# Kernel optimization log

Measured on AMD Instinct MI355X. Metric: run time of the kernel, lower is better.

The kernel has to match this reference:

```python
import jax, jax.numpy as jnp
import numpy as np

B, CIN, H, W = 4, 256, 56, 56
COUT, K = 256, 3
STRIDE, PAD, OG = 1, 1, 1
KK = K * K


def setup_inputs() -> dict:
    key = jax.random.key(0)
    k1, k2, k3, k4 = jax.random.split(key, 4)
    x = jax.random.normal(k1, (B, CIN, H, W), jnp.float32)
    # deformable conv weight [Cout, Cin/groups, K, K]
    weight = jax.random.normal(k2, (COUT, CIN, K, K), jnp.float32) * 0.05
    # offset-predicting 3x3 conv: 2*OG*K*K output channels (small init -> modest offsets)
    off_w = jax.random.normal(k3, (2 * OG * KK, CIN, 3, 3), jnp.float32) * 0.01
    off_b = jax.random.normal(k4, (2 * OG * KK,), jnp.float32) * 0.01
    return {"x": x, "weight": weight, "off_w": off_w, "off_b": off_b}


def _deform_conv(x, weight, off_w, off_b):
    Bn, C, Hh, Ww = x.shape
    # offset = param_generator(x): 3x3 conv, stride 1, pad 1
    offset = jax.lax.conv_general_dilated(
        x, off_w, window_strides=(1, 1), padding=((1, 1), (1, 1)),
        dimension_numbers=("NCHW", "OIHW", "NCHW")) + off_b[None, :, None, None]
    Ho = (Hh + 2 * PAD - K) // STRIDE + 1
    Wo = (Ww + 2 * PAD - K) // STRIDE + 1
    # torchvision layout: [B, OG, KK, (dy,dx), Ho, Wo]
    off = offset.reshape(Bn, OG, KK, 2, Ho, Wo)

    kh = jnp.arange(KK) // K
    kw = jnp.arange(KK) % K
    base_y = (jnp.arange(Ho) * STRIDE - PAD)[None, :, None] + kh[:, None, None]  # [KK,Ho,1]
    base_x = (jnp.arange(Wo) * STRIDE - PAD)[None, None, :] + kw[:, None, None]  # [KK,1,Wo]
    py = base_y[None, None].astype(x.dtype) + off[:, :, :, 0]  # [B,OG,KK,Ho,Wo]
    px = base_x[None, None].astype(x.dtype) + off[:, :, :, 1]

    Cg = C // OG
    xg = x.reshape(Bn, OG, Cg, Hh * Ww)

    def gather(yc, xc, wgt):
        # zero-padded bilinear corner: out-of-bounds samples contribute 0
        valid = (yc >= 0) & (yc < Hh) & (xc >= 0) & (xc < Ww)
        idx = (jnp.clip(yc, 0, Hh - 1) * Ww + jnp.clip(xc, 0, Ww - 1)).reshape(Bn, OG, 1, -1)
        v = jnp.take_along_axis(xg, idx, axis=3)            # [B,OG,Cg,KK*Ho*Wo]
        w = (wgt * valid.astype(wgt.dtype)).reshape(Bn, OG, 1, -1)
        return v * w

    y0 = jnp.floor(py).astype(jnp.int32)
    x0 = jnp.floor(px).astype(jnp.int32)
    ty = py - y0
    tx = px - x0
    sampled = (gather(y0,     x0,     (1 - ty) * (1 - tx))
             + gather(y0,     x0 + 1, (1 - ty) * tx)
             + gather(y0 + 1, x0,     ty * (1 - tx))
             + gather(y0 + 1, x0 + 1, ty * tx))
    sampled = sampled.reshape(Bn, C, KK, Ho, Wo)
    # weighted accumulation: implicit GEMM over (Cin, KK)
    return jnp.einsum("bikhw,oik->bohw", sampled, weight.reshape(COUT, C, KK))


def reference(x, weight, off_w, off_b):
    return _deform_conv(x, weight, off_w, off_b)
```

## Files before the change

kernel.cpp:

```cpp
#include <hip/hip_runtime.h>
#include <hip/hip_bf16.h>

#define B_N   4
#define CIN_  256
#define HH_   56
#define WW_   56
#define COUT_ 256
#define KK_   9
#define HW_   3136
#define KDIM  2304
#define NOFF  (B_N*18*HW_)
#define NOUT  (B_N*COUT_*HW_)

typedef __attribute__((ext_vector_type(8))) short short8;
typedef __attribute__((ext_vector_type(4))) float float4v;

__device__ __forceinline__ short f2bf_bits(float v) {
    union { __hip_bfloat16 h; short s; } u;
    u.h = __float2bfloat16(v);
    return u.s;
}
__device__ __forceinline__ float bfbits2f(short s) {
    union { unsigned u; float f; } u2;
    u2.u = ((unsigned)(unsigned short)s) << 16;
    return u2.f;
}

#define NB_AT  2304
#define NB_XT  784
#define NB_OW3 288
__global__ __launch_bounds__(256) void k_front(const float* __restrict__ x,
                                               const float* __restrict__ wgt,
                                               const float* __restrict__ ow,
                                               short* __restrict__ At2,
                                               short* __restrict__ xTb,
                                               short* __restrict__ owT3) {
    __shared__ float tile[64][65];
    int bx = blockIdx.x;
    int t = threadIdx.x;
    if (bx < NB_AT) {
        int i = bx*256 + t;
        int e = i & 7;
        int l = (i >> 3) & 63;
        int gg = i >> 9;
        int g  = gg % 72;
        int rt = gg / 72;
        int m = rt*16 + (l & 15);
        int k = g*32 + (l >> 4)*8 + e;
        int kk = k >> 8;  int ci = k & 255;
        At2[i] = f2bf_bits(wgt[(size_t)(m*CIN_ + ci)*9 + kk]);
        return;
    }
    if (bx < NB_AT + NB_XT) {
        int g = bx - NB_AT;
        int b = g / 196; int r = g % 196;
        int c0 = (r / 49) * 64; int p0 = (r % 49) * 64;
        int tp = t & 63;  int tc = t >> 6;
        #pragma unroll
        for (int i = 0; i < 16; ++i) {
            int ci = tc*16 + i;
            tile[ci][tp] = x[((size_t)b*CIN_ + c0 + ci)*HW_ + p0 + tp];
        }
        __syncthreads();
        #pragma unroll
        for (int i = 0; i < 16; ++i) {
            int p = tc*16 + i;
            xTb[((size_t)b*HW_ + p0 + p)*CIN_ + c0 + tp] = f2bf_bits(tile[tp][p]);
        }
        return;
    }
    {
        int i = (bx - NB_AT - NB_XT)*256 + t;
        int c = i / KDIM; int r = i % KDIM;
        int kk = r >> 8;  int ci = r & 255;
        owT3[i] = (c < 18) ? f2bf_bits(ow[(size_t)(c*CIN_ + ci)*9 + kk]) : 0;
    }
}

__global__ __launch_bounds__(256) void k_offgemm(const short* __restrict__ owT3,
                                                 const short* __restrict__ xTb,
                                                 float* __restrict__ pOff2) {
    __shared__ short sA[32*64];
    __shared__ short sB[64*64];
    __shared__ int   sP2[3*64];
    int t = threadIdx.x;
    int posb = blockIdx.x * 64;
    int b    = blockIdx.y;
    int ks   = blockIdx.z;
    int kt0  = ks * 768;
    int kend = kt0 + 768;

    for (int e = t; e < 3*64; e += 256) {
        int kk = ks*3 + (e >> 6); int row = e & 63;
        int pos = posb + row;
        int h = pos / WW_, w = pos % WW_;
        int yy = h + kk/3 - 1, xx = w + kk%3 - 1;
        bool v = (yy >= 0) && (yy < HH_) && (xx >= 0) && (xx < WW_);
        sP2[e] = v ? (yy*WW_ + xx) : -1;
    }
    __syncthreads();

    int arow = t >> 3,  aq  = t & 7;
    int brow = t >> 2,  bqc = (t & 3) * 2;

    int wv = t >> 6;
    int wm = (wv >> 1) * 16;
    int wn = (wv & 1) * 32;
    int lane = t & 63;
    int lm = lane & 15;
    int qd = lane >> 4;

    float4v acc[2];
    acc[0] = (float4v)(0.f); acc[1] = (float4v)(0.f);

    const short* gA = owT3 + (size_t)arow*KDIM + aq*8;
    const short* xb = xTb + (size_t)b*HW_*CIN_;

    short* wA = sA + (((arow >> 4)*8 + aq)*16 + ((arow + 2*aq) & 15))*8;
    short* wB[2];
    #pragma unroll
    for (int j = 0; j < 2; ++j) {
        int qq = bqc + j;
        wB[j] = sB + (((brow >> 4)*8 + qq)*16 + ((brow + 2*qq) & 15))*8;
    }

    short8 pa, pb[2];
    const short8 zero8 = (short8)(0);
    pa = *(const short8*)(gA + kt0);
    {
        int p2 = sP2[brow];
        #pragma unroll
        for (int j = 0; j < 2; ++j) {
            int ci0 = (kt0 & 255) + (bqc + j)*8;
            pb[j] = (p2 >= 0) ? *(const short8*)(xb + (size_t)p2*CIN_ + ci0) : zero8;
        }
    }

    for (int kt = kt0; kt < kend; kt += 64) {
        __syncthreads();
        *(short8*)wA = pa;
        #pragma unroll
        for (int j = 0; j < 2; ++j) *(short8*)wB[j] = pb[j];
        __syncthreads();
        int kt2 = kt + 64;
        if (kt2 < kend) {
            pa = *(const short8*)(gA + kt2);
            int kkl = (kt2 >> 8) - ks*3;
            int p2 = sP2[kkl*64 + brow];
            int cb = kt2 & 255;
            #pragma unroll
            for (int j = 0; j < 2; ++j) {
                int ci0 = cb + (bqc + j)*8;
                pb[j] = (p2 >= 0) ? *(const short8*)(xb + (size_t)p2*CIN_ + ci0) : zero8;
            }
        }
        #pragma unroll
        for (int kss = 0; kss < 2; ++kss) {
            int qe = kss*4 + qd;
            int sw = (lm + 2*qe) & 15;
            short8 af, bf[2];
            af = *(short8*)(sA + ((((wm>>4))*8 + qe)*16 + sw)*8);
            #pragma unroll
            for (int j = 0; j < 2; ++j)
                bf[j] = *(short8*)(sB + ((((wn>>4) + j)*8 + qe)*16 + sw)*8);
            #pragma unroll
            for (int j = 0; j < 2; ++j)
                acc[j] = __builtin_amdgcn_mfma_f32_16x16x32_bf16(
                             af, bf[j], acc[j], 0, 0, 0);
        }
    }

    float* pbase = pOff2 + (size_t)ks*NOFF;
    #pragma unroll
    for (int j = 0; j < 2; ++j) {
        int col = posb + wn + j*16 + lm;
        #pragma unroll
        for (int r = 0; r < 4; ++r) {
            int c = wm + qd*4 + r;
            if (c < 18)
                pbase[((size_t)(b*18 + c))*HW_ + col] = acc[j][r];
        }
    }
}

__global__ __launch_bounds__(256) void k_gemm(const short* __restrict__ At2,
                                              const short* __restrict__ xTb,
                                              const float* __restrict__ pOff2,
                                              const float* __restrict__ ob,
                                              float* __restrict__ pout) {
    __shared__ short sB[64*64];
    __shared__ int4   sPI[3*64];
    __shared__ float4 sPW[3*64];
    int t = threadIdx.x;

    int idx = blockIdx.x;
    int xcd = idx & 7;
    int b   = xcd & 3;
    int q   = (idx >> 3)*2 + (xcd >> 2);
    int m0   = (q & 1) * 128;
    int r2   = q >> 1;
    int posb = (r2 % 49) * 64;
    int ks   = r2 / 49;

    for (int e = t; e < 3*64; e += 256) {
        int kk = ks*3 + (e >> 6); int pl = e & 63;
        int pos = posb + pl;
        int h = pos / WW_, w = pos % WW_;
        size_t oy = (size_t)(b*18 + 2*kk    )*HW_ + pos;
        size_t ox = (size_t)(b*18 + 2*kk + 1)*HW_ + pos;
        float dy = ob[2*kk], dx = ob[2*kk + 1];
        #pragma unroll
        for (int s = 0; s < 3; ++s) {
            dy += pOff2[(size_t)s*NOFF + oy];
            dx += pOff2[(size_t)s*NOFF + ox];
        }
        float py = (float)(h - 1 + kk/3) + dy;
        float px = (float)(w - 1 + kk%3) + dx;
        float y0f = floorf(py), x0f = floorf(px);
        int y0 = (int)y0f, x0 = (int)x0f;
        float ty = py - y0f, tx = px - x0f;
        bool vy0 = (y0   >= 0) && (y0   < HH_);
        bool vy1 = (y0+1 >= 0) && (y0+1 < HH_);
        bool vx0 = (x0   >= 0) && (x0   < WW_);
        bool vx1 = (x0+1 >= 0) && (x0+1 < WW_);
        int y0c = min(max(y0,   0), HH_-1), y1c = min(max(y0+1, 0), HH_-1);
        int x0c = min(max(x0,   0), WW_-1), x1c = min(max(x0+1, 0), WW_-1);
        sPI[e] = make_int4(y0c*WW_+x0c, y0c*WW_+x1c, y1c*WW_+x0c, y1c*WW_+x1c);
        sPW[e] = make_float4((vy0 && vx0) ? (1.f-ty)*(1.f-tx) : 0.f,
                             (vy0 && vx1) ? (1.f-ty)*tx       : 0.f,
                             (vy1 && vx0) ? ty*(1.f-tx)       : 0.f,
                             (vy1 && vx1) ? ty*tx             : 0.f);
    }
    __syncthreads();

    int brow = t >> 2,  bqc = (t & 3) * 2;

    int wv = t >> 6;
    int wm = (wv >> 1) * 64;
    int wn = (wv & 1) * 32;
    int lane = t & 63;
    int lm = lane & 15;
    int qd = lane >> 4;

    float4v acc[4][2];
    #pragma unroll
    for (int i = 0; i < 4; ++i)
        #pragma unroll
        for (int j = 0; j < 2; ++j) acc[i][j] = (float4v)(0.f);

    const short* xb = xTb + (size_t)b*HW_*CIN_;
    const short* pA = At2 + (((size_t)((m0 + wm) >> 4) * 72) << 9) + (size_t)lane * 8;
    int g0 = ks * 24;

    short* wB[2];
    #pragma unroll
    for (int j = 0; j < 2; ++j) {
        int qq = bqc + j;
        wB[j] = sB + (((brow >> 4)*8 + qq)*16 + ((brow + 2*qq) & 15))*8;
    }

    short8 cg[2][4];
    float4 bwv;

#define CGLOAD(itX) do {                                                      \
    int4 id_ = sPI[((itX) >> 2)*64 + brow];                                   \
    bwv = sPW[((itX) >> 2)*64 + brow];                                        \
    int cb_ = ((itX) & 3) * 64;                                               \
    _Pragma("unroll")                                                         \
    for (int j = 0; j < 2; ++j) {                                             \
        int ci0_ = cb_ + (bqc + j)*8;                                         \
        cg[j][0] = *(const short8*)(xb + (size_t)id_.x*CIN_ + ci0_);          \
        cg[j][1] = *(const short8*)(xb + (size_t)id_.y*CIN_ + ci0_);          \
        cg[j][2] = *(const short8*)(xb + (size_t)id_.z*CIN_ + ci0_);          \
        cg[j][3] = *(const short8*)(xb + (size_t)id_.w*CIN_ + ci0_);          \
    }                                                                         \
} while (0)

    CGLOAD(0);

    for (int it = 0; it < 12; ++it) {
        short8 af[8];
        #pragma unroll
        for (int kss = 0; kss < 2; ++kss)
            #pragma unroll
            for (int i = 0; i < 4; ++i)
                af[kss*4 + i] = *(const short8*)(
                    pA + ((size_t)(i*72 + g0 + it*2 + kss) << 9));

        short8 pk[2];
        #pragma unroll
        for (int j = 0; j < 2; ++j) {
            float f[8];
            #pragma unroll
            for (int e = 0; e < 8; ++e)
                f[e] = bwv.x*bfbits2f(cg[j][0][e]) + bwv.y*bfbits2f(cg[j][1][e])
                     + bwv.z*bfbits2f(cg[j][2][e]) + bwv.w*bfbits2f(cg[j][3][e]);
            union { short8 s8; __hip_bfloat162 h2[4]; } pu;
            #pragma unroll
            for (int e2 = 0; e2 < 4; ++e2)
                pu.h2[e2] = __float22bfloat162_rn(make_float2(f[2*e2], f[2*e2+1]));
            pk[j] = pu.s8;
        }
        __syncthreads();
        #pragma unroll
        for (int j = 0; j < 2; ++j) *(short8*)wB[j] = pk[j];
        __syncthreads();
        if (it + 1 < 12) CGLOAD(it + 1);

        #pragma unroll
        for (int kss = 0; kss < 2; ++kss) {
            int qe = kss*4 + qd;
            int sw = (lm + 2*qe) & 15;
            short8 bf[2];
            #pragma unroll
            for (int j = 0; j < 2; ++j)
                bf[j] = *(short8*)(sB + ((((wn>>4) + j)*8 + qe)*16 + sw)*8);
            #pragma unroll
            for (int i = 0; i < 4; ++i)
                #pragma unroll
                for (int j = 0; j < 2; ++j)
                    acc[i][j] = __builtin_amdgcn_mfma_f32_16x16x32_bf16(
                                    af[kss*4 + i], bf[j], acc[i][j], 0, 0, 0);
        }
    }
#undef CGLOAD

    float* pbase = pout + (size_t)ks*NOUT;
    #pragma unroll
    for (int i = 0; i < 4; ++i)
        #pragma unroll
        for (int j = 0; j < 2; ++j) {
            int col = posb + wn + j*16 + lm;
            #pragma unroll
            for (int r = 0; r < 4; ++r) {
                int m = m0 + wm + i*16 + qd*4 + r;
                pbase[((size_t)b*COUT_ + m)*HW_ + col] = acc[i][j][r];
            }
        }
}

__global__ __launch_bounds__(256) void k_oreduce(const float* __restrict__ pout,
                                                 float* __restrict__ out) {
    int i = blockIdx.x*256 + threadIdx.x;
    if (i >= NOUT/4) return;
    float4 a = ((const float4*)pout)[i];
    float4 b = ((const float4*)(pout + NOUT))[i];
    float4 c = ((const float4*)(pout + 2*(size_t)NOUT))[i];
    float4 r;
    r.x = a.x + b.x + c.x;  r.y = a.y + b.y + c.y;
    r.z = a.z + b.z + c.z;  r.w = a.w + b.w + c.w;
    ((float4*)out)[i] = r;
}

extern "C" void kernel_launch(void* const* d_in, const int* in_sizes, int n_in,
                              void* d_out, int out_size, void* d_ws, size_t ws_size,
                              hipStream_t stream) {
    const float* x   = (const float*)d_in[0];
    const float* wgt = (const float*)d_in[1];
    const float* ow  = (const float*)d_in[2];
    const float* ob  = (const float*)d_in[3];
    float* out = (float*)d_out;

    char* ws = (char*)d_ws;
    short* At2   = (short*)ws;
    short* xTb   = (short*)(ws + 1179648);
    short* owT3  = (short*)(ws + 7602176);
    float* pOff2 = (float*)(ws + 7749632);
    float* pout  = (float*)(ws + 10459136);

    k_front  <<<dim3(NB_AT + NB_XT + NB_OW3), 256, 0, stream>>>(x, wgt, ow, At2, xTb, owT3);
    k_offgemm<<<dim3(49, 4, 3),               256, 0, stream>>>(owT3, xTb, pOff2);
    k_gemm   <<<dim3(1176),                   256, 0, stream>>>(At2, xTb, pOff2, ob, pout);
    k_oreduce<<<dim3(NOUT/4/256),             256, 0, stream>>>(pout, out);
}
```

Baseline: 128.8 us.

## Retile deform GEMM to full 256 Cout by 32 positions per block

Each block now covers all 256 output channels over 32 spatial positions, instead of 128 channels over 64 positions. The bilinear gather of sampled input columns therefore happens once per position rather than once per Cout half, which removes duplicated gather and interpolation work and its global loads. In exchange each block stages a smaller B tile, and the A (weight) fragments for all 256 rows are read by every block. The grid size stays the same, while per-thread gather work per iteration is halved.

Result: faster. 124.2 us (-3.6%).

```diff
diff --git a/kernel.cpp b/kernel.cpp
--- a/kernel.cpp
+++ b/kernel.cpp
@@ -188,22 +188,21 @@
                                               const float* __restrict__ pOff2,
                                               const float* __restrict__ ob,
                                               float* __restrict__ pout) {
-    __shared__ short sB[64*64];
-    __shared__ int4   sPI[3*64];
-    __shared__ float4 sPW[3*64];
+    __shared__ short sB[32*64];
+    __shared__ int4   sPI[3*32];
+    __shared__ float4 sPW[3*32];
     int t = threadIdx.x;
 
     int idx = blockIdx.x;
     int xcd = idx & 7;
     int b   = xcd & 3;
     int q   = (idx >> 3)*2 + (xcd >> 2);
-    int m0   = (q & 1) * 128;
-    int r2   = q >> 1;
-    int posb = (r2 % 49) * 64;
-    int ks   = r2 / 49;
-
-    for (int e = t; e < 3*64; e += 256) {
-        int kk = ks*3 + (e >> 6); int pl = e & 63;
+    int sidx = q % 98;
+    int ks   = q / 98;
+    int posb = sidx * 32;
+
+    for (int e = t; e < 3*32; e += 256) {
+        int kk = ks*3 + (e >> 5); int pl = e & 31;
         int pos = posb + pl;
         int h = pos / WW_, w = pos % WW_;
         size_t oy = (size_t)(b*18 + 2*kk    )*HW_ + pos;
@@ -233,11 +232,10 @@
     }
     __syncthreads();
 
-    int brow = t >> 2,  bqc = (t & 3) * 2;
+    int brow = t >> 3;
+    int bq   = t & 7;
 
     int wv = t >> 6;
-    int wm = (wv >> 1) * 64;
-    int wn = (wv & 1) * 32;
     int lane = t & 63;
     int lm = lane & 15;
     int qd = lane >> 4;
@@ -249,31 +247,22 @@
         for (int j = 0; j < 2; ++j) acc[i][j] = (float4v)(0.f);
 
     const short* xb = xTb + (size_t)b*HW_*CIN_;
-    const short* pA = At2 + (((size_t)((m0 + wm) >> 4) * 72) << 9) + (size_t)lane * 8;
+    const short* pA = At2 + (((size_t)(wv*4) * 72) << 9) + (size_t)lane * 8;
     int g0 = ks * 24;
 
-    short* wB[2];
-    #pragma unroll
-    for (int j = 0; j < 2; ++j) {
-        int qq = bqc + j;
-        wB[j] = sB + (((brow >> 4)*8 + qq)*16 + ((brow + 2*qq) & 15))*8;
-    }
-
-    short8 cg[2][4];
+    short* wB = sB + (((brow >> 4)*8 + bq)*16 + ((brow + 2*bq) & 15))*8;
+
+    short8 cg[4];
     float4 bwv;
 
 #define CGLOAD(itX) do {                                                      \
-    int4 id_ = sPI[((itX) >> 2)*64 + brow];                                   \
-    bwv = sPW[((itX) >> 2)*64 + brow];                                        \
-    int cb_ = ((itX) & 3) * 64;                                               \
-    _Pragma("unroll")                                                         \
-    for (int j = 0; j < 2; ++j) {                                             \
-        int ci0_ = cb_ + (bqc + j)*8;                                         \
-        cg[j][0] = *(const short8*)(xb + (size_t)id_.x*CIN_ + ci0_);          \
-        cg[j][1] = *(const short8*)(xb + (size_t)id_.y*CIN_ + ci0_);          \
-        cg[j][2] = *(const short8*)(xb + (size_t)id_.z*CIN_ + ci0_);          \
-        cg[j][3] = *(const short8*)(xb + (size_t)id_.w*CIN_ + ci0_);          \
-    }                                                                         \
+    int4 id_ = sPI[((itX) >> 2)*32 + brow];                                   \
+    bwv = sPW[((itX) >> 2)*32 + brow];                                        \
+    int ci0_ = ((itX) & 3) * 64 + bq*8;                                       \
+    cg[0] = *(const short8*)(xb + (size_t)id_.x*CIN_ + ci0_);                 \
+    cg[1] = *(const short8*)(xb + (size_t)id_.y*CIN_ + ci0_);                 \
+    cg[2] = *(const short8*)(xb + (size_t)id_.z*CIN_ + ci0_);                 \
+    cg[3] = *(const short8*)(xb + (size_t)id_.w*CIN_ + ci0_);                 \
 } while (0)
 
     CGLOAD(0);
@@ -287,23 +276,21 @@
                 af[kss*4 + i] = *(const short8*)(
                     pA + ((size_t)(i*72 + g0 + it*2 + kss) << 9));
 
-        short8 pk[2];
-        #pragma unroll
-        for (int j = 0; j < 2; ++j) {
+        short8 pk;
+        {
             float f[8];
             #pragma unroll
             for (int e = 0; e < 8; ++e)
-                f[e] = bwv.x*bfbits2f(cg[j][0][e]) + bwv.y*bfbits2f(cg[j][1][e])
-                     + bwv.z*bfbits2f(cg[j][2][e]) + bwv.w*bfbits2f(cg[j][3][e]);
+                f[e] = bwv.x*bfbits2f(cg[0][e]) + bwv.y*bfbits2f(cg[1][e])
+                     + bwv.z*bfbits2f(cg[2][e]) + bwv.w*bfbits2f(cg[3][e]);
             union { short8 s8; __hip_bfloat162 h2[4]; } pu;
             #pragma unroll
             for (int e2 = 0; e2 < 4; ++e2)
                 pu.h2[e2] = __float22bfloat162_rn(make_float2(f[2*e2], f[2*e2+1]));
-            pk[j] = pu.s8;
-        }
-        __syncthreads();
-        #pragma unroll
-        for (int j = 0; j < 2; ++j) *(short8*)wB[j] = pk[j];
+            pk = pu.s8;
+        }
+        __syncthreads();
+        *(short8*)wB = pk;
         __syncthreads();
         if (it + 1 < 12) CGLOAD(it + 1);
 
@@ -314,7 +301,7 @@
             short8 bf[2];
             #pragma unroll
             for (int j = 0; j < 2; ++j)
-                bf[j] = *(short8*)(sB + ((((wn>>4) + j)*8 + qe)*16 + sw)*8);
+                bf[j] = *(short8*)(sB + ((j*8 + qe)*16 + sw)*8);
             #pragma unroll
             for (int i = 0; i < 4; ++i)
                 #pragma unroll
@@ -330,10 +317,10 @@
     for (int i = 0; i < 4; ++i)
         #pragma unroll
         for (int j = 0; j < 2; ++j) {
-            int col = posb + wn + j*16 + lm;
+            int col = posb + j*16 + lm;
             #pragma unroll
             for (int r = 0; r < 4; ++r) {
-                int m = m0 + wm + i*16 + qd*4 + r;
+                int m = wv*64 + i*16 + qd*4 + r;
                 pbase[((size_t)b*COUT_ + m)*HW_ + col] = acc[i][j][r];
             }
         }
```
